# Kernel optimization log

Hardware: AMD Instinct MI355X
Metric: run time of the kernel (lower is better)

## Reference

```python
import jax, jax.numpy as jnp
import numpy as np

B, N, T_OBS, N_HEAD, D = 4, 2048, 8, 4, 16  # D = t_obs*2 = in/out feat of GAT
S, NSAMP = 2, 20
OUT_DIM = S * NSAMP  # 40
SEG = 64  # pedestrians per scene -> 32 scenes, block-diagonal mask


def _xavier(key, shape, gain=1.414):
    fan_in, fan_out = shape[-2], shape[-1]
    a = gain * np.sqrt(6.0 / (fan_in + fan_out))
    return jax.random.uniform(key, shape, jnp.float32, -a, a)


def setup_inputs() -> dict:
    key = jax.random.key(0)
    ks = jax.random.split(key, 12)
    x = jax.random.normal(ks[0], (B, N, T_OBS, 2), jnp.float32)
    # block-diagonal scene mask: 32 scenes of 64 peds each
    scene_id = jnp.arange(N) // SEG
    mask = (scene_id[:, None] == scene_id[None, :]).astype(jnp.float32)
    w = _xavier(ks[1], (N_HEAD, D, D))
    a_src = _xavier(ks[2], (N_HEAD, D, 1))
    a_dst = _xavier(ks[3], (N_HEAD, D, 1))
    bias = jnp.zeros((D,), jnp.float32)
    # MLP dims: (16,) + (16, 64) + (40,)
    W1 = _xavier(ks[4], (D, 16), gain=1.0)
    b1 = jnp.zeros((16,), jnp.float32)
    W2 = _xavier(ks[5], (16, 64), gain=1.0)
    b2 = jnp.zeros((64,), jnp.float32)
    W3 = _xavier(ks[6], (64, OUT_DIM), gain=1.0)
    b3 = jnp.zeros((OUT_DIM,), jnp.float32)
    return {"x": x, "mask": mask, "w": w, "a_src": a_src, "a_dst": a_dst,
            "bias": bias, "W1": W1, "b1": b1, "W2": W2, "b2": b2, "W3": W3, "b3": b3}


def reference(x, mask, w, a_src, a_dst, bias, W1, b1, W2, b2, W3, b3):
    b, n = x.shape[0], x.shape[1]
    node = x.reshape(b, n, -1)                       # (B, N, 16)
    # GAT
    hp = jnp.einsum('bni,hio->bhno', node, w)        # (B, H, N, D)
    attn_src = jnp.einsum('bhno,hoe->bhne', hp, a_src)[..., 0]  # (B, H, N)
    attn_dst = jnp.einsum('bhno,hoe->bhne', hp, a_dst)[..., 0]  # (B, H, N)
    attn = attn_src[:, :, :, None] * attn_dst[:, :, None, :]    # (B, H, N, N)
    attn = jnp.where(attn >= 0, attn, 0.2 * attn)    # leaky_relu(0.2)
    attn = jax.nn.softmax(attn, axis=-1)             # softmax over full row
    attn = attn * mask                                # mask AFTER softmax (as in source)
    out = jnp.einsum('bhnm,bhmo->bno', attn, hp) + bias
    out = out + hp.sum(axis=1)                        # skip connection
    # MLP head: activation applied BEFORE each Linear (per source), dropout disabled
    y = jax.nn.relu(out) @ W1 + b1
    y = jax.nn.relu(y) @ W2 + b2
    y = jax.nn.relu(y) @ W3 + b3
    y = y.reshape(b, n, NSAMP, -1)[..., 0:S]          # (B, N, 20, 2)
    return jnp.clip(jax.nn.sigmoid(y), 0.01, 0.99)
```

## Files before the change

### kernel.cpp

```cpp
#include <hip/hip_runtime.h>
#include <math.h>

#define L2E 1.4426950408889634f

#if defined(__has_builtin)
#if __has_builtin(__builtin_amdgcn_exp2f)
#define EXP2F(x) __builtin_amdgcn_exp2f(x)
#else
#define EXP2F(x) exp2f(x)
#endif
#else
#define EXP2F(x) exp2f(x)
#endif

__global__ __launch_bounds__(512, 4) void k_fused(
    const float* __restrict__ x, const float* __restrict__ w,
    const float* __restrict__ a_src, const float* __restrict__ a_dst,
    const float* __restrict__ bias,
    const float* __restrict__ W1, const float* __restrict__ b1,
    const float* __restrict__ W2, const float* __restrict__ b2,
    const float* __restrict__ W3, const float* __restrict__ b3,
    float* __restrict__ out)
{
    __shared__ __align__(16) float RA[8192];
    __shared__ __align__(16) float RB[2112];
    __shared__ __align__(16) float RC[5120];
    __shared__ float cs_v[4][16], cd_v[4][16];
    __shared__ float s_v[64];
    __shared__ float me_v[64], den_v[64];
    __shared__ float mxs[8][4], mns[8][4];
    __shared__ float pden[8 * 64];
    __shared__ float feat[16][17];

    const int t = threadIdx.x;
    const int b  = blockIdx.x >> 7;
    const int sc = (blockIdx.x >> 2) & 31;
    const int qt = blockIdx.x & 3;
    const int n0 = sc * 64;
    const int r0 = n0 + qt * 16;

    {
        const float* xb = x + ((size_t)b * 2048 + n0) * 16;
        int u0 = t, u1 = t + 512;
        RB[(u0 >> 4) * 17 + (u0 & 15)] = xb[u0];
        RB[(u1 >> 4) * 17 + (u1 & 15)] = xb[u1];
    }
    RB[1088 + t] = w[t];
    RB[1600 + t] = w[512 + t];
    if (t < 128) {
        int h = t >> 5, which = (t >> 4) & 1, i = t & 15;
        const float* av = which ? (a_dst + h * 16) : (a_src + h * 16);
        float acc = 0.f;
        #pragma unroll
        for (int o = 0; o < 16; ++o) acc = fmaf(w[h * 256 + i * 16 + o], av[o], acc);
        float* cv = which ? &cd_v[0][0] : &cs_v[0][0];
        cv[h * 16 + i] = acc;
    }
    __syncthreads();

    {
        const float4* xb = (const float4*)(x + (size_t)b * 2048 * 16);
        #pragma unroll
        for (int rep = 0; rep < 4; ++rep) {
            int n = t + rep * 512;
            float4 x0 = xb[n * 4 + 0], x1 = xb[n * 4 + 1];
            float4 x2 = xb[n * 4 + 2], x3 = xb[n * 4 + 3];
            float xr[16] = {x0.x,x0.y,x0.z,x0.w, x1.x,x1.y,x1.z,x1.w,
                            x2.x,x2.y,x2.z,x2.w, x3.x,x3.y,x3.z,x3.w};
            float dh[4];
            #pragma unroll
            for (int h = 0; h < 4; ++h) {
                float acc = 0.f;
                #pragma unroll
                for (int i = 0; i < 16; ++i) acc = fmaf(xr[i], cd_v[h][i], acc);
                dh[h] = acc;
            }
            ((float4*)RA)[n] = make_float4(dh[0], dh[1], dh[2], dh[3]);
        }
    }
    if (t < 64) {
        int h = t >> 4, k = t & 15;
        float acc = 0.f;
        #pragma unroll
        for (int i = 0; i < 16; ++i)
            acc = fmaf(RB[(qt * 16 + k) * 17 + i], cs_v[h][i], acc);
        s_v[h * 16 + k] = acc;
    }
    #pragma unroll
    for (int rep = 0; rep < 2; ++rep) {
        int u = t + rep * 512;
        int h = u >> 8, m = (u >> 2) & 63, oq = u & 3;
        float a0 = 0.f, a1 = 0.f, a2 = 0.f, a3 = 0.f;
        #pragma unroll
        for (int i = 0; i < 16; ++i) {
            float xv = RB[m * 17 + i];
            const float* wr = &RB[1088 + h * 256 + i * 16 + oq * 4];
            a0 = fmaf(xv, wr[0], a0);
            a1 = fmaf(xv, wr[1], a1);
            a2 = fmaf(xv, wr[2], a2);
            a3 = fmaf(xv, wr[3], a3);
        }
        ((float4*)RC)[(h * 64 + m) * 5 + oq] = make_float4(a0, a1, a2, a3);
    }
    __syncthreads();

    {
        const float4* d4 = (const float4*)RA;
        float4 v0 = d4[t * 4 + 0], v1 = d4[t * 4 + 1];
        float4 v2 = d4[t * 4 + 2], v3 = d4[t * 4 + 3];
        float mx0 = fmaxf(fmaxf(v0.x, v1.x), fmaxf(v2.x, v3.x));
        float mx1 = fmaxf(fmaxf(v0.y, v1.y), fmaxf(v2.y, v3.y));
        float mx2 = fmaxf(fmaxf(v0.z, v1.z), fmaxf(v2.z, v3.z));
        float mx3 = fmaxf(fmaxf(v0.w, v1.w), fmaxf(v2.w, v3.w));
        float mn0 = fminf(fminf(v0.x, v1.x), fminf(v2.x, v3.x));
        float mn1 = fminf(fminf(v0.y, v1.y), fminf(v2.y, v3.y));
        float mn2 = fminf(fminf(v0.z, v1.z), fminf(v2.z, v3.z));
        float mn3 = fminf(fminf(v0.w, v1.w), fminf(v2.w, v3.w));
        #pragma unroll
        for (int off = 32; off >= 1; off >>= 1) {
            mx0 = fmaxf(mx0, __shfl_xor(mx0, off));
            mx1 = fmaxf(mx1, __shfl_xor(mx1, off));
            mx2 = fmaxf(mx2, __shfl_xor(mx2, off));
            mx3 = fmaxf(mx3, __shfl_xor(mx3, off));
            mn0 = fminf(mn0, __shfl_xor(mn0, off));
            mn1 = fminf(mn1, __shfl_xor(mn1, off));
            mn2 = fminf(mn2, __shfl_xor(mn2, off));
            mn3 = fminf(mn3, __shfl_xor(mn3, off));
        }
        if ((t & 63) == 0) {
            int wv = t >> 6;
            mxs[wv][0] = mx0; mxs[wv][1] = mx1; mxs[wv][2] = mx2; mxs[wv][3] = mx3;
            mns[wv][0] = mn0; mns[wv][1] = mn1; mns[wv][2] = mn2; mns[wv][3] = mn3;
        }
    }
    __syncthreads();

    {
        int wv = t >> 6, L = t & 63;
        int h = L >> 4;
        float dmax = mxs[0][h], dmin = mns[0][h];
        #pragma unroll
        for (int wq = 1; wq < 8; ++wq) {
            dmax = fmaxf(dmax, mxs[wq][h]);
            dmin = fminf(dmin, mns[wq][h]);
        }
        float LP = fmaxf(dmax, 0.2f * dmax);
        float LN = fminf(dmin, 0.2f * dmin);
        float s  = s_v[L];
        float me_nat = (s >= 0.f) ? s * LP : s * LN;
        float nme = -me_nat * L2E;
        float sL = s * L2E, s2L = 0.2f * sL;
        if (wv == 0) me_v[L] = nme;
        const float* dcol = RA + wv * 1024 + h;
        float a0 = 0.f, a1 = 0.f, a2 = 0.f, a3 = 0.f;
        #pragma unroll 4
        for (int c = 0; c < 256; c += 4) {
            float d0 = dcol[(c + 0) * 4];
            float d1 = dcol[(c + 1) * 4];
            float d2 = dcol[(c + 2) * 4];
            float d3 = dcol[(c + 3) * 4];
            a0 += EXP2F(fmaxf(fmaf(sL, d0, nme), fmaf(s2L, d0, nme)));
            a1 += EXP2F(fmaxf(fmaf(sL, d1, nme), fmaf(s2L, d1, nme)));
            a2 += EXP2F(fmaxf(fmaf(sL, d2, nme), fmaf(s2L, d2, nme)));
            a3 += EXP2F(fmaxf(fmaf(sL, d3, nme), fmaf(s2L, d3, nme)));
        }
        pden[wv * 64 + L] = (a0 + a1) + (a2 + a3);
    }
    __syncthreads();
    if (t < 64) {
        float s = 0.f;
        #pragma unroll
        for (int wq = 0; wq < 8; ++wq) s += pden[wq * 64 + t];
        den_v[t] = s;
    }
    __syncthreads();

    {
        int wv = t >> 6, L = t & 63;
        int h = wv >> 1;
        int kk = (wv & 1) * 8 + (L >> 3);
        int p = L & 7;
        int row = h * 16 + kk;
        float s = s_v[row];
        float sL = s * L2E, s2L = 0.2f * sL;
        float nme = me_v[row];
        float inv = 1.0f / den_v[row];
        float a[16];
        #pragma unroll
        for (int i = 0; i < 16; ++i) a[i] = 0.f;
        #pragma unroll
        for (int c = 0; c < 8; ++c) {
            int m = c * 8 + p;
            float d = RA[(n0 + m) * 4 + h];
            float e = fmaxf(fmaf(sL, d, nme), fmaf(s2L, d, nme));
            float pr = EXP2F(e) * inv;
            const float4* hr = ((const float4*)RC) + (h * 64 + m) * 5;
            float4 h0 = hr[0], h1 = hr[1], h2 = hr[2], h3 = hr[3];
            a[0]  = fmaf(pr, h0.x, a[0]);  a[1]  = fmaf(pr, h0.y, a[1]);
            a[2]  = fmaf(pr, h0.z, a[2]);  a[3]  = fmaf(pr, h0.w, a[3]);
            a[4]  = fmaf(pr, h1.x, a[4]);  a[5]  = fmaf(pr, h1.y, a[5]);
            a[6]  = fmaf(pr, h1.z, a[6]);  a[7]  = fmaf(pr, h1.w, a[7]);
            a[8]  = fmaf(pr, h2.x, a[8]);  a[9]  = fmaf(pr, h2.y, a[9]);
            a[10] = fmaf(pr, h2.z, a[10]); a[11] = fmaf(pr, h2.w, a[11]);
            a[12] = fmaf(pr, h3.x, a[12]); a[13] = fmaf(pr, h3.y, a[13]);
            a[14] = fmaf(pr, h3.z, a[14]); a[15] = fmaf(pr, h3.w, a[15]);
        }
        #pragma unroll
        for (int i = 0; i < 16; ++i) {
            a[i] += __shfl_xor(a[i], 1);
            a[i] += __shfl_xor(a[i], 2);
            a[i] += __shfl_xor(a[i], 4);
        }
        if (p == 0) {
            float* po = &RB[(h * 16 + kk) * 16];
            #pragma unroll
            for (int i = 0; i < 16; ++i) po[i] = a[i];
        }
    }
    __syncthreads();

    #pragma unroll
    for (int rep = 0; rep < 5; ++rep) RA[1360 + t + rep * 512] = W3[t + rep * 512];
    RA[272 + t] = W2[t];
    RA[784 + t] = W2[512 + t];
    if (t < 256) RA[t] = W1[t];
    if (t < 16) RA[256 + t] = b1[t];
    else if (t >= 32 && t < 96) RA[1296 + (t - 32)] = b2[t - 32];
    else if (t >= 96 && t < 136) RA[3920 + (t - 96)] = b3[t - 96];
    if (t < 256) {
        int k = t >> 4, i = t & 15;
        float v = bias[i];
        #pragma unroll
        for (int h = 0; h < 4; ++h)
            v += RB[(h * 16 + k) * 16 + i] + RC[(h * 64 + qt * 16 + k) * 20 + i];
        feat[k][i] = v;
    }
    __syncthreads();

    if (t < 256) {
        int k = t >> 4, j = t & 15;
        float acc = RA[256 + j];
        #pragma unroll
        for (int i = 0; i < 16; ++i)
            acc = fmaf(fmaxf(feat[k][i], 0.f), RA[i * 16 + j], acc);
        RC[k * 17 + j] = acc;
    }
    __syncthreads();

    {
        int k = t >> 5, g = t & 31;
        float acc0 = RA[1296 + g * 2], acc1 = RA[1296 + g * 2 + 1];
        #pragma unroll
        for (int j = 0; j < 16; ++j) {
            float r = fmaxf(RC[k * 17 + j], 0.f);
            acc0 = fmaf(r, RA[272 + j * 64 + g * 2], acc0);
            acc1 = fmaf(r, RA[272 + j * 64 + g * 2 + 1], acc1);
        }
        RC[544 + k * 65 + g * 2]     = acc0;
        RC[544 + k * 65 + g * 2 + 1] = acc1;
    }
    __syncthreads();

    for (int idx = t; idx < 640; idx += 512) {
        int k = idx / 40, c = idx % 40;
        float acc = RA[3920 + c];
        #pragma unroll 8
        for (int q = 0; q < 64; ++q)
            acc = fmaf(fmaxf(RC[544 + k * 65 + q], 0.f), RA[1360 + q * 40 + c], acc);
        float v = 1.0f / (1.0f + EXP2F(-acc * L2E));
        v = fminf(fmaxf(v, 0.01f), 0.99f);
        out[((size_t)(b * 2048) + r0 + k) * 40 + c] = v;
    }
}

extern "C" void kernel_launch(void* const* d_in, const int* in_sizes, int n_in,
                              void* d_out, int out_size, void* d_ws, size_t ws_size,
                              hipStream_t stream) {
    (void)in_sizes; (void)n_in; (void)out_size; (void)d_ws; (void)ws_size;
    const float* x     = (const float*)d_in[0];
    const float* w     = (const float*)d_in[2];
    const float* a_src = (const float*)d_in[3];
    const float* a_dst = (const float*)d_in[4];
    const float* bias  = (const float*)d_in[5];
    const float* W1    = (const float*)d_in[6];
    const float* b1    = (const float*)d_in[7];
    const float* W2    = (const float*)d_in[8];
    const float* b2    = (const float*)d_in[9];
    const float* W3    = (const float*)d_in[10];
    const float* b3    = (const float*)d_in[11];
    float* outp = (float*)d_out;

    hipLaunchKernelGGL(k_fused, dim3(512), dim3(512), 0, stream,
                       x, w, a_src, a_dst, bias, W1, b1, W2, b2, W3, b3, outp);
}
```

Measured before the change: 35.54 us.

## Split projection into separate kernel writing hp, src and dst scores to workspace

The fused kernel is split in two. A small first kernel computes the per-head projections hp and the source and destination attention scores once, writing them to global workspace. The second kernel loads these precomputed values instead of having each of the 512 blocks recompute the destination scores for all 2048 nodes. It also stores the destination scores per head in a padded head-major layout for float4 reads. This adds a second launch and a global round trip of about 2.2 MB, and a stray `dS[0]=dS[0]` write is left in the load loop.

```diff
diff --git a/kernel.cpp b/kernel.cpp
--- a/kernel.cpp
+++ b/kernel.cpp
@@ -13,23 +13,68 @@
 #define EXP2F(x) exp2f(x)
 #endif
 
-__global__ __launch_bounds__(512, 4) void k_fused(
+#define WS_HP 0
+#define WS_D  524288
+#define WS_S  557056
+
+__global__ __launch_bounds__(128) void k_proj(
     const float* __restrict__ x, const float* __restrict__ w,
     const float* __restrict__ a_src, const float* __restrict__ a_dst,
-    const float* __restrict__ bias,
+    float* __restrict__ ws)
+{
+    __shared__ float w_s[256], as_s[16], ad_s[16];
+    int t = threadIdx.x;
+    int bh = blockIdx.x >> 4, tile = blockIdx.x & 15;
+    int h = bh & 3, b = bh >> 2;
+    int n = tile * 128 + t;
+    w_s[t] = w[h * 256 + t];
+    w_s[128 + t] = w[h * 256 + 128 + t];
+    if (t < 16) { as_s[t] = a_src[h * 16 + t]; ad_s[t] = a_dst[h * 16 + t]; }
+    __syncthreads();
+
+    const float4* xp = (const float4*)(x + ((size_t)b * 2048 + n) * 16);
+    float4 x0 = xp[0], x1 = xp[1], x2 = xp[2], x3 = xp[3];
+    float nv[16] = {x0.x,x0.y,x0.z,x0.w, x1.x,x1.y,x1.z,x1.w,
+                    x2.x,x2.y,x2.z,x2.w, x3.x,x3.y,x3.z,x3.w};
+    float acc[16];
+    #pragma unroll
+    for (int o = 0; o < 16; ++o) acc[o] = 0.f;
+    #pragma unroll
+    for (int i = 0; i < 16; ++i) {
+        float ni = nv[i];
+        #pragma unroll
+        for (int o = 0; o < 16; ++o) acc[o] = fmaf(ni, w_s[i * 16 + o], acc[o]);
+    }
+    float sv = 0.f, dv = 0.f;
+    #pragma unroll
+    for (int o = 0; o < 16; ++o) {
+        sv = fmaf(acc[o], as_s[o], sv);
+        dv = fmaf(acc[o], ad_s[o], dv);
+    }
+    float4* hp4 = (float4*)(ws + WS_HP);
+    size_t base = ((size_t)bh * 2048 + n) * 4;
+    hp4[base + 0] = make_float4(acc[0],  acc[1],  acc[2],  acc[3]);
+    hp4[base + 1] = make_float4(acc[4],  acc[5],  acc[6],  acc[7]);
+    hp4[base + 2] = make_float4(acc[8],  acc[9],  acc[10], acc[11]);
+    hp4[base + 3] = make_float4(acc[12], acc[13], acc[14], acc[15]);
+    ws[WS_D + bh * 2048 + n] = dv;
+    ws[WS_S + bh * 2048 + n] = sv;
+}
+
+#define DLD 2052
+__global__ __launch_bounds__(512, 4) void k_scene(
+    const float* __restrict__ ws, const float* __restrict__ bias,
     const float* __restrict__ W1, const float* __restrict__ b1,
     const float* __restrict__ W2, const float* __restrict__ b2,
     const float* __restrict__ W3, const float* __restrict__ b3,
     float* __restrict__ out)
 {
-    __shared__ __align__(16) float RA[8192];
-    __shared__ __align__(16) float RB[2112];
+    __shared__ __align__(16) float dS[4 * DLD];
     __shared__ __align__(16) float RC[5120];
-    __shared__ float cs_v[4][16], cd_v[4][16];
-    __shared__ float s_v[64];
-    __shared__ float me_v[64], den_v[64];
-    __shared__ float mxs[8][4], mns[8][4];
-    __shared__ float pden[8 * 64];
+    __shared__ __align__(16) float RB[1024];
+    __shared__ float pden[512];
+    __shared__ float s_v[64], me_v[64], den_v[64];
+    __shared__ float mxs[8], mns[8];
     __shared__ float feat[16][17];
 
     const int t = threadIdx.x;
@@ -40,129 +85,69 @@
     const int r0 = n0 + qt * 16;
 
     {
-        const float* xb = x + ((size_t)b * 2048 + n0) * 16;
-        int u0 = t, u1 = t + 512;
-        RB[(u0 >> 4) * 17 + (u0 & 15)] = xb[u0];
-        RB[(u1 >> 4) * 17 + (u1 & 15)] = xb[u1];
-    }
-    RB[1088 + t] = w[t];
-    RB[1600 + t] = w[512 + t];
-    if (t < 128) {
-        int h = t >> 5, which = (t >> 4) & 1, i = t & 15;
-        const float* av = which ? (a_dst + h * 16) : (a_src + h * 16);
-        float acc = 0.f;
-        #pragma unroll
-        for (int o = 0; o < 16; ++o) acc = fmaf(w[h * 256 + i * 16 + o], av[o], acc);
-        float* cv = which ? &cd_v[0][0] : &cs_v[0][0];
-        cv[h * 16 + i] = acc;
-    }
-    __syncthreads();
-
-    {
-        const float4* xb = (const float4*)(x + (size_t)b * 2048 * 16);
+        const float4* gd = (const float4*)(ws + WS_D + (size_t)b * 4 * 2048);
         #pragma unroll
         for (int rep = 0; rep < 4; ++rep) {
-            int n = t + rep * 512;
-            float4 x0 = xb[n * 4 + 0], x1 = xb[n * 4 + 1];
-            float4 x2 = xb[n * 4 + 2], x3 = xb[n * 4 + 3];
-            float xr[16] = {x0.x,x0.y,x0.z,x0.w, x1.x,x1.y,x1.z,x1.w,
-                            x2.x,x2.y,x2.z,x2.w, x3.x,x3.y,x3.z,x3.w};
-            float dh[4];
-            #pragma unroll
-            for (int h = 0; h < 4; ++h) {
-                float acc = 0.f;
-                #pragma unroll
-                for (int i = 0; i < 16; ++i) acc = fmaf(xr[i], cd_v[h][i], acc);
-                dh[h] = acc;
-            }
-            ((float4*)RA)[n] = make_float4(dh[0], dh[1], dh[2], dh[3]);
-        }
-    }
-    if (t < 64) {
-        int h = t >> 4, k = t & 15;
-        float acc = 0.f;
-        #pragma unroll
-        for (int i = 0; i < 16; ++i)
-            acc = fmaf(RB[(qt * 16 + k) * 17 + i], cs_v[h][i], acc);
-        s_v[h * 16 + k] = acc;
-    }
-    #pragma unroll
-    for (int rep = 0; rep < 2; ++rep) {
-        int u = t + rep * 512;
-        int h = u >> 8, m = (u >> 2) & 63, oq = u & 3;
-        float a0 = 0.f, a1 = 0.f, a2 = 0.f, a3 = 0.f;
-        #pragma unroll
-        for (int i = 0; i < 16; ++i) {
-            float xv = RB[m * 17 + i];
-            const float* wr = &RB[1088 + h * 256 + i * 16 + oq * 4];
-            a0 = fmaf(xv, wr[0], a0);
-            a1 = fmaf(xv, wr[1], a1);
-            a2 = fmaf(xv, wr[2], a2);
-            a3 = fmaf(xv, wr[3], a3);
-        }
-        ((float4*)RC)[(h * 64 + m) * 5 + oq] = make_float4(a0, a1, a2, a3);
-    }
-    __syncthreads();
-
-    {
-        const float4* d4 = (const float4*)RA;
-        float4 v0 = d4[t * 4 + 0], v1 = d4[t * 4 + 1];
-        float4 v2 = d4[t * 4 + 2], v3 = d4[t * 4 + 3];
-        float mx0 = fmaxf(fmaxf(v0.x, v1.x), fmaxf(v2.x, v3.x));
-        float mx1 = fmaxf(fmaxf(v0.y, v1.y), fmaxf(v2.y, v3.y));
-        float mx2 = fmaxf(fmaxf(v0.z, v1.z), fmaxf(v2.z, v3.z));
-        float mx3 = fmaxf(fmaxf(v0.w, v1.w), fmaxf(v2.w, v3.w));
-        float mn0 = fminf(fminf(v0.x, v1.x), fminf(v2.x, v3.x));
-        float mn1 = fminf(fminf(v0.y, v1.y), fminf(v2.y, v3.y));
-        float mn2 = fminf(fminf(v0.z, v1.z), fminf(v2.z, v3.z));
-        float mn3 = fminf(fminf(v0.w, v1.w), fminf(v2.w, v3.w));
+            int u = t + rep * 512;
+            int h = u >> 9, j4 = u & 511;
+            ((float4*)dS)[h * (DLD / 4) + j4] = gd[h * 512 + j4];
+        }
+        const float4* gh = (const float4*)(ws + WS_HP);
+        #pragma unroll
+        for (int rep = 0; rep < 2; ++rep) {
+            int u = t + rep * 512;
+            int h = u >> 8, m = (u >> 2) & 63, q = u & 3;
+            float4 v = gh[((size_t)(b * 4 + h) * 2048 + n0 + m) * 4 + q];
+            dS[0] = dS[0];
+            *(float4*)&RC[(h * 64 + m) * 20 + q * 4] = v;
+        }
+        if (t < 64) {
+            int h = t >> 4, k = t & 15;
+            s_v[t] = ws[WS_S + (size_t)(b * 4 + h) * 2048 + r0 + k];
+        }
+    }
+    __syncthreads();
+
+    {
+        int h = t >> 7, idx = t & 127;
+        const float4* d4 = (const float4*)dS + h * (DLD / 4);
+        float mx = -3.4e38f, mn = 3.4e38f;
+        #pragma unroll
+        for (int rep = 0; rep < 4; ++rep) {
+            float4 v = d4[idx + rep * 128];
+            mx = fmaxf(mx, fmaxf(fmaxf(v.x, v.y), fmaxf(v.z, v.w)));
+            mn = fminf(mn, fminf(fminf(v.x, v.y), fminf(v.z, v.w)));
+        }
         #pragma unroll
         for (int off = 32; off >= 1; off >>= 1) {
-            mx0 = fmaxf(mx0, __shfl_xor(mx0, off));
-            mx1 = fmaxf(mx1, __shfl_xor(mx1, off));
-            mx2 = fmaxf(mx2, __shfl_xor(mx2, off));
-            mx3 = fmaxf(mx3, __shfl_xor(mx3, off));
-            mn0 = fminf(mn0, __shfl_xor(mn0, off));
-            mn1 = fminf(mn1, __shfl_xor(mn1, off));
-            mn2 = fminf(mn2, __shfl_xor(mn2, off));
-            mn3 = fminf(mn3, __shfl_xor(mn3, off));
-        }
-        if ((t & 63) == 0) {
-            int wv = t >> 6;
-            mxs[wv][0] = mx0; mxs[wv][1] = mx1; mxs[wv][2] = mx2; mxs[wv][3] = mx3;
-            mns[wv][0] = mn0; mns[wv][1] = mn1; mns[wv][2] = mn2; mns[wv][3] = mn3;
-        }
+            mx = fmaxf(mx, __shfl_xor(mx, off));
+            mn = fminf(mn, __shfl_xor(mn, off));
+        }
+        if ((t & 63) == 0) { int wv = t >> 6; mxs[wv] = mx; mns[wv] = mn; }
     }
     __syncthreads();
 
     {
         int wv = t >> 6, L = t & 63;
         int h = L >> 4;
-        float dmax = mxs[0][h], dmin = mns[0][h];
-        #pragma unroll
-        for (int wq = 1; wq < 8; ++wq) {
-            dmax = fmaxf(dmax, mxs[wq][h]);
-            dmin = fminf(dmin, mns[wq][h]);
-        }
+        float dmax = fmaxf(mxs[2 * h], mxs[2 * h + 1]);
+        float dmin = fminf(mns[2 * h], mns[2 * h + 1]);
         float LP = fmaxf(dmax, 0.2f * dmax);
         float LN = fminf(dmin, 0.2f * dmin);
-        float s  = s_v[L];
+        float s = s_v[L];
         float me_nat = (s >= 0.f) ? s * LP : s * LN;
         float nme = -me_nat * L2E;
         float sL = s * L2E, s2L = 0.2f * sL;
         if (wv == 0) me_v[L] = nme;
-        const float* dcol = RA + wv * 1024 + h;
+        const float4* dcol = (const float4*)dS + h * (DLD / 4) + wv * 64;
         float a0 = 0.f, a1 = 0.f, a2 = 0.f, a3 = 0.f;
-        #pragma unroll 4
-        for (int c = 0; c < 256; c += 4) {
-            float d0 = dcol[(c + 0) * 4];
-            float d1 = dcol[(c + 1) * 4];
-            float d2 = dcol[(c + 2) * 4];
-            float d3 = dcol[(c + 3) * 4];
-            a0 += EXP2F(fmaxf(fmaf(sL, d0, nme), fmaf(s2L, d0, nme)));
-            a1 += EXP2F(fmaxf(fmaf(sL, d1, nme), fmaf(s2L, d1, nme)));
-            a2 += EXP2F(fmaxf(fmaf(sL, d2, nme), fmaf(s2L, d2, nme)));
-            a3 += EXP2F(fmaxf(fmaf(sL, d3, nme), fmaf(s2L, d3, nme)));
+        #pragma unroll 8
+        for (int c = 0; c < 64; ++c) {
+            float4 dv = dcol[c];
+            a0 += EXP2F(fmaxf(fmaf(sL, dv.x, nme), fmaf(s2L, dv.x, nme)));
+            a1 += EXP2F(fmaxf(fmaf(sL, dv.y, nme), fmaf(s2L, dv.y, nme)));
+            a2 += EXP2F(fmaxf(fmaf(sL, dv.z, nme), fmaf(s2L, dv.z, nme)));
+            a3 += EXP2F(fmaxf(fmaf(sL, dv.w, nme), fmaf(s2L, dv.w, nme)));
         }
         pden[wv * 64 + L] = (a0 + a1) + (a2 + a3);
     }
@@ -191,7 +176,7 @@
         #pragma unroll
         for (int c = 0; c < 8; ++c) {
             int m = c * 8 + p;
-            float d = RA[(n0 + m) * 4 + h];
+            float d = dS[h * DLD + n0 + m];
             float e = fmaxf(fmaf(sL, d, nme), fmaf(s2L, d, nme));
             float pr = EXP2F(e) * inv;
             const float4* hr = ((const float4*)RC) + (h * 64 + m) * 5;
@@ -220,13 +205,13 @@
     __syncthreads();
 
     #pragma unroll
-    for (int rep = 0; rep < 5; ++rep) RA[1360 + t + rep * 512] = W3[t + rep * 512];
-    RA[272 + t] = W2[t];
-    RA[784 + t] = W2[512 + t];
-    if (t < 256) RA[t] = W1[t];
-    if (t < 16) RA[256 + t] = b1[t];
-    else if (t >= 32 && t < 96) RA[1296 + (t - 32)] = b2[t - 32];
-    else if (t >= 96 && t < 136) RA[3920 + (t - 96)] = b3[t - 96];
+    for (int rep = 0; rep < 5; ++rep) dS[1360 + t + rep * 512] = W3[t + rep * 512];
+    dS[272 + t] = W2[t];
+    dS[784 + t] = W2[512 + t];
+    if (t < 256) dS[t] = W1[t];
+    if (t < 16) dS[256 + t] = b1[t];
+    else if (t >= 32 && t < 96) dS[1296 + (t - 32)] = b2[t - 32];
+    else if (t >= 96 && t < 136) dS[3920 + (t - 96)] = b3[t - 96];
     if (t < 256) {
         int k = t >> 4, i = t & 15;
         float v = bias[i];
@@ -239,22 +224,22 @@
 
     if (t < 256) {
         int k = t >> 4, j = t & 15;
-        float acc = RA[256 + j];
+        float acc = dS[256 + j];
         #pragma unroll
         for (int i = 0; i < 16; ++i)
-            acc = fmaf(fmaxf(feat[k][i], 0.f), RA[i * 16 + j], acc);
+            acc = fmaf(fmaxf(feat[k][i], 0.f), dS[i * 16 + j], acc);
         RC[k * 17 + j] = acc;
     }
     __syncthreads();
 
     {
         int k = t >> 5, g = t & 31;
-        float acc0 = RA[1296 + g * 2], acc1 = RA[1296 + g * 2 + 1];
+        float acc0 = dS[1296 + g * 2], acc1 = dS[1296 + g * 2 + 1];
         #pragma unroll
         for (int j = 0; j < 16; ++j) {
             float r = fmaxf(RC[k * 17 + j], 0.f);
-            acc0 = fmaf(r, RA[272 + j * 64 + g * 2], acc0);
-            acc1 = fmaf(r, RA[272 + j * 64 + g * 2 + 1], acc1);
+            acc0 = fmaf(r, dS[272 + j * 64 + g * 2], acc0);
+            acc1 = fmaf(r, dS[272 + j * 64 + g * 2 + 1], acc1);
         }
         RC[544 + k * 65 + g * 2]     = acc0;
         RC[544 + k * 65 + g * 2 + 1] = acc1;
@@ -263,10 +248,10 @@
 
     for (int idx = t; idx < 640; idx += 512) {
         int k = idx / 40, c = idx % 40;
-        float acc = RA[3920 + c];
+        float acc = dS[3920 + c];
         #pragma unroll 8
         for (int q = 0; q < 64; ++q)
-            acc = fmaf(fmaxf(RC[544 + k * 65 + q], 0.f), RA[1360 + q * 40 + c], acc);
+            acc = fmaf(fmaxf(RC[544 + k * 65 + q], 0.f), dS[1360 + q * 40 + c], acc);
         float v = 1.0f / (1.0f + EXP2F(-acc * L2E));
         v = fminf(fmaxf(v, 0.01f), 0.99f);
         out[((size_t)(b * 2048) + r0 + k) * 40 + c] = v;
@@ -276,7 +261,7 @@
 extern "C" void kernel_launch(void* const* d_in, const int* in_sizes, int n_in,
                               void* d_out, int out_size, void* d_ws, size_t ws_size,
                               hipStream_t stream) {
-    (void)in_sizes; (void)n_in; (void)out_size; (void)d_ws; (void)ws_size;
+    (void)in_sizes; (void)n_in; (void)out_size; (void)ws_size;
     const float* x     = (const float*)d_in[0];
     const float* w     = (const float*)d_in[2];
     const float* a_src = (const float*)d_in[3];
@@ -288,8 +273,11 @@
     const float* b2    = (const float*)d_in[9];
     const float* W3    = (const float*)d_in[10];
     const float* b3    = (const float*)d_in[11];
+    float* ws   = (float*)d_ws;
     float* outp = (float*)d_out;
 
-    hipLaunchKernelGGL(k_fused, dim3(512), dim3(512), 0, stream,
-                       x, w, a_src, a_dst, bias, W1, b1, W2, b2, W3, b3, outp);
+    hipLaunchKernelGGL(k_proj, dim3(256), dim3(128), 0, stream,
+                       x, w, a_src, a_dst, ws);
+    hipLaunchKernelGGL(k_scene, dim3(512), dim3(512), 0, stream,
+                       ws, bias, W1, b1, W2, b2, W3, b3, outp);
 }
```

Result: faster. 32.06 us (-9.8%).
